# Performance work log

Measured on AMD Instinct MI355X. Metric: run time of the kernel, lower is better.

## Reference

```python
import jax, jax.numpy as jnp
import numpy as np

N_NODES = 100000
N_EDGES = 1600000
D_IN = 264
D_HID = 64
NEG_SLOPE = 0.2


def _glorot(key, shape):
    fan_in, fan_out = shape[0], shape[-1]
    lim = jnp.sqrt(6.0 / (fan_in + fan_out))
    return jax.random.uniform(key, shape, jnp.float32, -lim, lim)


def setup_inputs() -> dict:
    key = jax.random.key(0)
    ks = jax.random.split(key, 24)
    x = jax.random.normal(ks[0], (N_NODES, D_IN), jnp.float32)
    src = jax.random.randint(ks[1], (N_EDGES,), 0, N_NODES, jnp.int32)
    off = jax.random.randint(ks[2], (N_EDGES,), 1, N_NODES, jnp.int32)
    dst = (src + off) % N_NODES  # guaranteed no self loops
    edge_index = jnp.stack([src, dst], axis=0)
    edge_attr = jax.random.normal(ks[3], (N_EDGES, 1), jnp.float32)
    p = {
        'l1_Wl': _glorot(ks[4], (D_IN, D_HID)), 'l1_bl': jnp.zeros((D_HID,), jnp.float32),
        'l1_Wr': _glorot(ks[5], (D_IN, D_HID)), 'l1_br': jnp.zeros((D_HID,), jnp.float32),
        'l1_We': _glorot(ks[6], (1, D_HID)),
        'l1_att': _glorot(ks[7], (1, 1, D_HID)), 'l1_bias': jnp.zeros((D_HID,), jnp.float32),
        'l2_Wl': _glorot(ks[8], (D_HID, D_HID)), 'l2_bl': jnp.zeros((D_HID,), jnp.float32),
        'l2_Wr': _glorot(ks[9], (D_HID, D_HID)), 'l2_br': jnp.zeros((D_HID,), jnp.float32),
        'l2_We': _glorot(ks[10], (1, D_HID)),
        'l2_att': _glorot(ks[11], (1, 1, D_HID)), 'l2_bias': jnp.zeros((D_HID,), jnp.float32),
        'W3': _glorot(ks[12], (D_HID, D_HID)), 'b3': jnp.zeros((D_HID,), jnp.float32),
        'W4': _glorot(ks[13], (D_HID, 1)), 'b4': jnp.zeros((1,), jnp.float32),
    }
    return dict(x=x, edge_index=edge_index, edge_attr=edge_attr, **p)


def _gatv2_layer(x, src, dst, ea, Wl, bl, Wr, br, We, att, bias):
    # heads=1, concat=True, aggr='max' (passed via **kwargs to MessagePassing)
    n = x.shape[0]
    xl = (x @ Wl + bl).reshape(n, 1, D_HID)  # source-side transform
    xr = (x @ Wr + br).reshape(n, 1, D_HID)  # target-side transform
    e = (ea @ We).reshape(-1, 1, D_HID)      # lin_edge, no bias
    m = jax.nn.leaky_relu(xr[dst] + xl[src] + e, NEG_SLOPE)  # (Etot,1,64)
    logits = jnp.sum(m * att, axis=-1)       # (Etot,1)
    # segment softmax over destination nodes
    mx = jax.ops.segment_max(logits, dst, num_segments=n)
    ex = jnp.exp(logits - mx[dst])
    den = jax.ops.segment_sum(ex, dst, num_segments=n)
    alpha = ex / den[dst]                    # (Etot,1)
    msg = xl[src] * alpha[:, :, None]        # (Etot,1,64)
    out = jax.ops.segment_max(msg, dst, num_segments=n)  # aggr='max'
    return out.reshape(n, D_HID) + bias


def _gcn_forward(x, src, dst, edge_attr,
                 l1_Wl, l1_bl, l1_Wr, l1_br, l1_We, l1_att, l1_bias,
                 l2_Wl, l2_bl, l2_Wr, l2_br, l2_We, l2_att, l2_bias,
                 W3, b3, W4, b4):
    n = x.shape[0]
    # add_self_loops with fill_value='mean' (edges contain no self loops)
    loop = jnp.arange(n, dtype=src.dtype)
    src2 = jnp.concatenate([src, loop])
    dst2 = jnp.concatenate([dst, loop])
    mean_ea = jnp.mean(edge_attr, axis=0, keepdims=True)  # (1,1)
    ea2 = jnp.concatenate([edge_attr, jnp.broadcast_to(mean_ea, (n, 1))], axis=0)
    h = _gatv2_layer(x, src2, dst2, ea2, l1_Wl, l1_bl, l1_Wr, l1_br, l1_We, l1_att, l1_bias)
    h = jax.nn.relu(h)  # dropout inactive in eval
    h = _gatv2_layer(h, src2, dst2, ea2, l2_Wl, l2_bl, l2_Wr, l2_br, l2_We, l2_att, l2_bias)
    h = jax.nn.relu(h)
    h = jax.nn.relu(h @ W3 + b3)
    h = h @ W4 + b4
    return jnp.squeeze(h, axis=-1)  # (N,)


def reference(x, edge_index, edge_attr,
              l1_Wl, l1_bl, l1_Wr, l1_br, l1_We, l1_att, l1_bias,
              l2_Wl, l2_bl, l2_Wr, l2_br, l2_We, l2_att, l2_bias,
              W3, b3, W4, b4):
    src, dst = edge_index[0], edge_index[1]
    return _gcn_forward(x, src, dst, edge_attr,
                        l1_Wl, l1_bl, l1_Wr, l1_br, l1_We, l1_att, l1_bias,
                        l2_Wl, l2_bl, l2_Wr, l2_br, l2_We, l2_att, l2_bias,
                        W3, b3, W4, b4)
```

## Files before the change

kernel.cpp:

```cpp
#include <hip/hip_runtime.h>
#include <math.h>
#include <float.h>

#define NN 100000
#define NE 1600000
#define ETOT 1700000
#define DIN 264
#define DH 64
#define SLOPE 0.2f
#define NB 98

typedef __attribute__((ext_vector_type(8))) short s8v;
typedef __attribute__((ext_vector_type(4))) float f4v;

__device__ __forceinline__ unsigned short f2bf(float x) {
  unsigned u = __float_as_uint(x);
  u += 0x7FFFu + ((u >> 16) & 1u);
  return (unsigned short)(u >> 16);
}
__device__ __forceinline__ float bf2f(unsigned short h) {
  return __uint_as_float(((unsigned)h) << 16);
}

__global__ void k_mean(const float* __restrict__ ea, float* __restrict__ sum) {
  float acc = 0.f;
  for (int i = blockIdx.x * blockDim.x + threadIdx.x; i < NE; i += gridDim.x * blockDim.x)
    acc += ea[i];
  #pragma unroll
  for (int off = 32; off > 0; off >>= 1) acc += __shfl_xor(acc, off);
  __shared__ float s[4];
  int lane = threadIdx.x & 63, w = threadIdx.x >> 6;
  if (lane == 0) s[w] = acc;
  __syncthreads();
  if (threadIdx.x == 0) atomicAdd(sum, s[0] + s[1] + s[2] + s[3]);
}

__global__ void k_hist(const int* __restrict__ ei, unsigned* __restrict__ deg) {
  int e = blockIdx.x * blockDim.x + threadIdx.x;
  if (e >= ETOT) return;
  int d = (e < NE) ? ei[NE + e] : e - NE;
  atomicAdd(&deg[d], 1u);
}

__global__ __launch_bounds__(256)
void k_bsum(const unsigned* __restrict__ deg, unsigned* __restrict__ bsum) {
  int i0 = blockIdx.x * 1024 + threadIdx.x * 4;
  unsigned s = 0;
  if (i0 + 3 < NN) {
    uint4 v = *(const uint4*)&deg[i0];
    s = v.x + v.y + v.z + v.w;
  }
  #pragma unroll
  for (int off = 32; off > 0; off >>= 1) s += __shfl_xor(s, off);
  __shared__ unsigned ws[4];
  int lane = threadIdx.x & 63, w = threadIdx.x >> 6;
  if (lane == 0) ws[w] = s;
  __syncthreads();
  if (threadIdx.x == 0) bsum[blockIdx.x] = ws[0] + ws[1] + ws[2] + ws[3];
}

__global__ __launch_bounds__(128)
void k_sscan(unsigned* __restrict__ bsum, unsigned* __restrict__ rowptr) {
  __shared__ unsigned ls[128];
  int t = threadIdx.x;
  unsigned v = (t < NB) ? bsum[t] : 0u;
  ls[t] = v;
  __syncthreads();
  for (int off = 1; off < 128; off <<= 1) {
    unsigned u = (t >= off) ? ls[t - off] : 0u;
    __syncthreads();
    ls[t] += u;
    __syncthreads();
  }
  if (t < NB) bsum[t] = ls[t] - v;
  if (t == 127) rowptr[NN] = ls[127];
}

__global__ __launch_bounds__(256)
void k_scan2(const unsigned* __restrict__ deg, const unsigned* __restrict__ bsum,
             unsigned* __restrict__ rowptr, unsigned* __restrict__ wptr) {
  __shared__ unsigned ls[256];
  int i0 = blockIdx.x * 1024 + threadIdx.x * 4;
  unsigned d0 = 0, d1 = 0, d2 = 0, d3 = 0;
  if (i0 + 3 < NN) {
    uint4 v = *(const uint4*)&deg[i0];
    d0 = v.x; d1 = v.y; d2 = v.z; d3 = v.w;
  }
  unsigned ts = d0 + d1 + d2 + d3;
  ls[threadIdx.x] = ts;
  __syncthreads();
  for (int off = 1; off < 256; off <<= 1) {
    unsigned u = (threadIdx.x >= (unsigned)off) ? ls[threadIdx.x - off] : 0u;
    __syncthreads();
    ls[threadIdx.x] += u;
    __syncthreads();
  }
  unsigned base = bsum[blockIdx.x] + ls[threadIdx.x] - ts;
  if (i0 + 3 < NN) {
    uint4 r;
    r.x = base;
    r.y = base + d0;
    r.z = r.y + d1;
    r.w = r.z + d2;
    *(uint4*)&rowptr[i0] = r;
    *(uint4*)&wptr[i0] = r;
  }
}

__global__ void k_scatter(const int* __restrict__ ei, const float* __restrict__ ea,
                          const float* __restrict__ sump, unsigned* __restrict__ wptr,
                          int2* __restrict__ csr) {
  int e = blockIdx.x * blockDim.x + threadIdx.x;
  if (e >= ETOT) return;
  int s, d;
  float a;
  if (e < NE) {
    s = ei[e];
    d = ei[NE + e];
    a = ea[e];
  } else {
    s = d = e - NE;
    a = sump[0] * (1.0f / NE);
  }
  unsigned pos = atomicAdd(&wptr[d], 1u);
  csr[pos] = make_int2(s, __float_as_int(a));
}

template <int K>
__global__ __launch_bounds__(256)
void k_wprep(const float* __restrict__ Wl, const float* __restrict__ Wr,
             unsigned short* __restrict__ wfh, unsigned short* __restrict__ wfl) {
  constexpr int KC = (K + 31) / 32;
  int t = blockIdx.x * blockDim.x + threadIdx.x;
  if (t >= 8 * KC * 64) return;
  int lane = t & 63;
  int kc = (t >> 6) % KC;
  int ntg = t / (64 * KC);
  const float* src = (ntg < 4) ? Wl : Wr;
  int n = (ntg & 3) * 16 + (lane & 15);
  int k0 = kc * 32 + (lane >> 4) * 8;
  #pragma unroll
  for (int i = 0; i < 8; i++) {
    int k = k0 + i;
    float v = (k < K) ? src[k * DH + n] : 0.f;
    unsigned short hh = f2bf(v);
    wfh[t * 8 + i] = hh;
    wfl[t * 8 + i] = f2bf(v - bf2f(hh));
  }
}

template <int K>
__global__ __launch_bounds__(512) __attribute__((amdgpu_waves_per_eu(4)))
void k_mm(const float* __restrict__ X,
          const unsigned short* __restrict__ wfh, const unsigned short* __restrict__ wfl,
          const float* __restrict__ bl, const float* __restrict__ br,
          float* __restrict__ xl, float* __restrict__ xr) {
  constexpr int KC = (K + 31) / 32;
  constexpr int KP = KC * 32;
  constexpr int SP = KP + 8;
  __shared__ unsigned short lsh[64 * SP];
  __shared__ unsigned short lsl[64 * SP];
  const int r0 = blockIdx.x * 64;
  const int tid = threadIdx.x;
  const int lane = tid & 63, w = tid >> 6;
  const int kq = lane >> 4;
  const int ar = lane & 15;

  s8v bh[KC], bv[KC];
  #pragma unroll
  for (int kc = 0; kc < KC; kc++) {
    const int bidx = ((w * KC + kc) * 64 + lane) * 8;
    bh[kc] = *(const s8v*)&wfh[bidx];
    bv[kc] = *(const s8v*)&wfl[bidx];
  }

  if constexpr (KP > K) {
    constexpr int PADW = (KP - K) / 2;
    for (int t = tid; t < 64 * PADW; t += 512) {
      int row = t / PADW, c = t - row * PADW;
      *(unsigned*)&lsh[row * SP + K + 2 * c] = 0u;
      *(unsigned*)&lsl[row * SP + K + 2 * c] = 0u;
    }
  }
  {
    constexpr int HK = K / 2;
    for (int p = tid; p < 64 * HK; p += 512) {
      int row = p / HK, kp = p - row * HK;
      int grow = r0 + row;
      float a = 0.f, b = 0.f;
      if (grow < NN) {
        float2 v = *(const float2*)&X[(size_t)grow * K + 2 * kp];
        a = v.x; b = v.y;
      }
      unsigned short ha = f2bf(a), hb = f2bf(b);
      unsigned short la = f2bf(a - bf2f(ha)), lb = f2bf(b - bf2f(hb));
      *(unsigned*)&lsh[row * SP + 2 * kp] = (unsigned)ha | ((unsigned)hb << 16);
      *(unsigned*)&lsl[row * SP + 2 * kp] = (unsigned)la | ((unsigned)lb << 16);
    }
  }
  __syncthreads();

  f4v acc[4];
  #pragma unroll
  for (int mt = 0; mt < 4; mt++) acc[mt] = (f4v){0.f, 0.f, 0.f, 0.f};
  #pragma unroll
  for (int kc = 0; kc < KC; kc++) {
    const int kb = kc * 32 + kq * 8;
    #pragma unroll
    for (int mt = 0; mt < 4; mt++) {
      s8v ah = *(const s8v*)&lsh[(mt * 16 + ar) * SP + kb];
      s8v al = *(const s8v*)&lsl[(mt * 16 + ar) * SP + kb];
      acc[mt] = __builtin_amdgcn_mfma_f32_16x16x32_bf16(ah, bh[kc], acc[mt], 0, 0, 0);
      acc[mt] = __builtin_amdgcn_mfma_f32_16x16x32_bf16(ah, bv[kc], acc[mt], 0, 0, 0);
      acc[mt] = __builtin_amdgcn_mfma_f32_16x16x32_bf16(al, bh[kc], acc[mt], 0, 0, 0);
    }
  }

  const float* bias = (w < 4) ? bl : br;
  float* outp = (w < 4) ? xl : xr;
  const int col = (w & 3) * 16 + ar;
  const float bvv = bias[col];
  #pragma unroll
  for (int mt = 0; mt < 4; mt++) {
    #pragma unroll
    for (int r = 0; r < 4; r++) {
      int grow = r0 + mt * 16 + kq * 4 + r;
      if (grow < NN) outp[(size_t)grow * DH + col] = acc[mt][r] + bvv;
    }
  }
}

template <bool HEAD>
__global__ void k_attn(const unsigned* __restrict__ rowptr, const int2* __restrict__ csr,
                       const float* __restrict__ xl, const float* __restrict__ xr,
                       const float* __restrict__ We, const float* __restrict__ att,
                       const float* __restrict__ bias, float* __restrict__ h,
                       const float* __restrict__ W3, const float* __restrict__ b3,
                       const float* __restrict__ W4, const float* __restrict__ b4,
                       float* __restrict__ out) {
  int n = (blockIdx.x * blockDim.x + threadIdx.x) >> 4;
  int l = threadIdx.x & 15;
  int g0 = threadIdx.x & 48;
  if (n >= NN) return;
  int l4 = l * 4;
  float4 xr4 = *(const float4*)&xr[n * DH + l4];
  float4 we4 = *(const float4*)&We[l4];
  float4 at4 = *(const float4*)&att[l4];
  int beg = rowptr[n], end = rowptr[n + 1];
  float M, D;
  float4 V;
  {
    int2 c0 = csr[beg];
    float a = __int_as_float(c0.y);
    float4 sl = *(const float4*)&xl[c0.x * DH + l4];
    float v, p = 0.f;
    v = xr4.x + sl.x + a * we4.x; v = v > 0.f ? v : SLOPE * v; p += v * at4.x;
    v = xr4.y + sl.y + a * we4.y; v = v > 0.f ? v : SLOPE * v; p += v * at4.y;
    v = xr4.z + sl.z + a * we4.z; v = v > 0.f ? v : SLOPE * v; p += v * at4.z;
    v = xr4.w + sl.w + a * we4.w; v = v > 0.f ? v : SLOPE * v; p += v * at4.w;
    p += __shfl_xor(p, 1);
    p += __shfl_xor(p, 2);
    p += __shfl_xor(p, 4);
    p += __shfl_xor(p, 8);
    M = p; D = 1.f; V = sl;
  }
  for (int e0 = beg + 1; e0 < end; e0 += 16) {
    int2 cl = csr[min(e0 + l, end - 1)];
    int cnt = min(16, end - e0);
    for (int i = 0; i < cnt; i += 4) {
      int mm = min(4, cnt - i);
      float4 sl[4];
      float av[4];
      #pragma unroll
      for (int j = 0; j < 4; j++) {
        if (j < mm) {
          int s = __shfl(cl.x, g0 + i + j);
          av[j] = __int_as_float(__shfl(cl.y, g0 + i + j));
          sl[j] = *(const float4*)&xl[s * DH + l4];
        }
      }
      #pragma unroll
      for (int j = 0; j < 4; j++) {
        if (j < mm) {
          float a = av[j];
          float v, p = 0.f;
          v = xr4.x + sl[j].x + a * we4.x; v = v > 0.f ? v : SLOPE * v; p += v * at4.x;
          v = xr4.y + sl[j].y + a * we4.y; v = v > 0.f ? v : SLOPE * v; p += v * at4.y;
          v = xr4.z + sl[j].z + a * we4.z; v = v > 0.f ? v : SLOPE * v; p += v * at4.z;
          v = xr4.w + sl[j].w + a * we4.w; v = v > 0.f ? v : SLOPE * v; p += v * at4.w;
          p += __shfl_xor(p, 1);
          p += __shfl_xor(p, 2);
          p += __shfl_xor(p, 4);
          p += __shfl_xor(p, 8);
          float Mn = fmaxf(M, p);
          float sO = __expf(M - Mn), sN = __expf(p - Mn);
          D = D * sO + sN;
          V.x = fmaxf(V.x * sO, sl[j].x * sN);
          V.y = fmaxf(V.y * sO, sl[j].y * sN);
          V.z = fmaxf(V.z * sO, sl[j].z * sN);
          V.w = fmaxf(V.w * sO, sl[j].w * sN);
          M = Mn;
        }
      }
    }
  }
  float inv = 1.0f / D;
  float4 b = *(const float4*)&bias[l4];
  float4 o;
  o.x = fmaxf(V.x * inv + b.x, 0.f);
  o.y = fmaxf(V.y * inv + b.y, 0.f);
  o.z = fmaxf(V.z * inv + b.z, 0.f);
  o.w = fmaxf(V.w * inv + b.w, 0.f);
  if (!HEAD) {
    *(float4*)&h[n * DH + l4] = o;
  } else {
    float4 acc = {0.f, 0.f, 0.f, 0.f};
    #pragma unroll
    for (int kk = 0; kk < 16; kk++) {
      float4 hk;
      hk.x = __shfl(o.x, g0 + kk);
      hk.y = __shfl(o.y, g0 + kk);
      hk.z = __shfl(o.z, g0 + kk);
      hk.w = __shfl(o.w, g0 + kk);
      float4 w0 = *(const float4*)&W3[(kk * 4 + 0) * DH + l4];
      acc.x = fmaf(hk.x, w0.x, acc.x);
      acc.y = fmaf(hk.x, w0.y, acc.y);
      acc.z = fmaf(hk.x, w0.z, acc.z);
      acc.w = fmaf(hk.x, w0.w, acc.w);
      float4 w1 = *(const float4*)&W3[(kk * 4 + 1) * DH + l4];
      acc.x = fmaf(hk.y, w1.x, acc.x);
      acc.y = fmaf(hk.y, w1.y, acc.y);
      acc.z = fmaf(hk.y, w1.z, acc.z);
      acc.w = fmaf(hk.y, w1.w, acc.w);
      float4 w2 = *(const float4*)&W3[(kk * 4 + 2) * DH + l4];
      acc.x = fmaf(hk.z, w2.x, acc.x);
      acc.y = fmaf(hk.z, w2.y, acc.y);
      acc.z = fmaf(hk.z, w2.z, acc.z);
      acc.w = fmaf(hk.z, w2.w, acc.w);
      float4 w3 = *(const float4*)&W3[(kk * 4 + 3) * DH + l4];
      acc.x = fmaf(hk.w, w3.x, acc.x);
      acc.y = fmaf(hk.w, w3.y, acc.y);
      acc.z = fmaf(hk.w, w3.z, acc.z);
      acc.w = fmaf(hk.w, w3.w, acc.w);
    }
    float4 b3v = *(const float4*)&b3[l4];
    float4 w4v = *(const float4*)&W4[l4];
    float t, p = 0.f;
    t = acc.x + b3v.x; t = t > 0.f ? t : 0.f; p += t * w4v.x;
    t = acc.y + b3v.y; t = t > 0.f ? t : 0.f; p += t * w4v.y;
    t = acc.z + b3v.z; t = t > 0.f ? t : 0.f; p += t * w4v.z;
    t = acc.w + b3v.w; t = t > 0.f ? t : 0.f; p += t * w4v.w;
    p += __shfl_xor(p, 1);
    p += __shfl_xor(p, 2);
    p += __shfl_xor(p, 4);
    p += __shfl_xor(p, 8);
    if (l == 0) out[n] = p + b4[0];
  }
}

extern "C" void kernel_launch(void* const* d_in, const int* in_sizes, int n_in,
                              void* d_out, int out_size, void* d_ws, size_t ws_size,
                              hipStream_t stream) {
  const float* x      = (const float*)d_in[0];
  const int*   ei     = (const int*)d_in[1];
  const float* ea     = (const float*)d_in[2];
  const float* l1_Wl  = (const float*)d_in[3];
  const float* l1_bl  = (const float*)d_in[4];
  const float* l1_Wr  = (const float*)d_in[5];
  const float* l1_br  = (const float*)d_in[6];
  const float* l1_We  = (const float*)d_in[7];
  const float* l1_att = (const float*)d_in[8];
  const float* l1_bias= (const float*)d_in[9];
  const float* l2_Wl  = (const float*)d_in[10];
  const float* l2_bl  = (const float*)d_in[11];
  const float* l2_Wr  = (const float*)d_in[12];
  const float* l2_br  = (const float*)d_in[13];
  const float* l2_We  = (const float*)d_in[14];
  const float* l2_att = (const float*)d_in[15];
  const float* l2_bias= (const float*)d_in[16];
  const float* W3     = (const float*)d_in[17];
  const float* b3     = (const float*)d_in[18];
  const float* W4     = (const float*)d_in[19];
  const float* b4     = (const float*)d_in[20];
  float* out = (float*)d_out;

  float*    ws     = (float*)d_ws;
  float*    sum    = ws;
  float*    xl     = ws + 256;
  float*    xr     = xl + NN * DH;
  float*    h      = xr + NN * DH;
  int2*     csr    = (int2*)(h + NN * DH);
  unsigned* rowptr = (unsigned*)(csr + ETOT);
  unsigned* wptr   = rowptr + NN + 4;
  unsigned* deg    = wptr + NN;
  unsigned* bsum   = deg + NN;
  unsigned short* wf1h = (unsigned short*)(bsum + 128);
  unsigned short* wf1l = wf1h + 36864;
  unsigned short* wf2h = wf1l + 36864;
  unsigned short* wf2l = wf2h + 8192;

  const int B = 256;
  const int mm_blocks   = (NN + 63) / 64;
  const int edge_blocks = (ETOT + B - 1) / B;
  const int attn_blocks = (NN * 16) / B;

  hipMemsetAsync(sum, 0, 256 * sizeof(float), stream);
  hipMemsetAsync(deg, 0, NN * sizeof(unsigned), stream);
  k_wprep<DIN><<<(8 * 9 * 64 + B - 1) / B, B, 0, stream>>>(l1_Wl, l1_Wr, wf1h, wf1l);
  k_wprep<DH><<<(8 * 2 * 64 + B - 1) / B, B, 0, stream>>>(l2_Wl, l2_Wr, wf2h, wf2l);
  k_mean<<<256, B, 0, stream>>>(ea, sum);
  k_hist<<<edge_blocks, B, 0, stream>>>(ei, deg);
  k_bsum<<<NB, B, 0, stream>>>(deg, bsum);
  k_sscan<<<1, 128, 0, stream>>>(bsum, rowptr);
  k_scan2<<<NB, B, 0, stream>>>(deg, bsum, rowptr, wptr);
  k_scatter<<<edge_blocks, B, 0, stream>>>(ei, ea, sum, wptr, csr);

  k_mm<DIN><<<mm_blocks, 512, 0, stream>>>(x, wf1h, wf1l, l1_bl, l1_br, xl, xr);
  k_attn<false><<<attn_blocks, B, 0, stream>>>(rowptr, csr, xl, xr, l1_We, l1_att,
                                               l1_bias, h, W3, b3, W4, b4, out);

  k_mm<DH><<<mm_blocks, 512, 0, stream>>>(h, wf2h, wf2l, l2_bl, l2_br, xl, xr);
  k_attn<true><<<attn_blocks, B, 0, stream>>>(rowptr, csr, xl, xr, l2_We, l2_att,
                                              l2_bias, h, W3, b3, W4, b4, out);
}
```

Measured before the change: 661.9 us.

## Shard histogram and CSR scatter atomics by destination range across blocks

The histogram and scatter kernels now launch NSHARD copies of each edge chunk. Each block handles only the destinations in its shard's node range, and blockIdx.x interleaves the shards. The aim is to confine the atomics from concurrently running blocks to separate address ranges, improving L2 locality and spreading atomic contention on MI355X's partitioned caches. In exchange, every block reads the destination indices eight times, and most threads do no work after filtering.

```diff
diff --git a/kernel.cpp b/kernel.cpp
--- a/kernel.cpp
+++ b/kernel.cpp
@@ -9,6 +9,9 @@
 #define DH 64
 #define SLOPE 0.2f
 #define NB 98
+#define NSHARD 8
+#define SHW 12500
+#define EPB 2048
 
 typedef __attribute__((ext_vector_type(8))) short s8v;
 typedef __attribute__((ext_vector_type(4))) float f4v;
@@ -35,11 +38,20 @@
   if (threadIdx.x == 0) atomicAdd(sum, s[0] + s[1] + s[2] + s[3]);
 }
 
-__global__ void k_hist(const int* __restrict__ ei, unsigned* __restrict__ deg) {
-  int e = blockIdx.x * blockDim.x + threadIdx.x;
-  if (e >= ETOT) return;
-  int d = (e < NE) ? ei[NE + e] : e - NE;
-  atomicAdd(&deg[d], 1u);
+__global__ __launch_bounds__(256)
+void k_hist(const int* __restrict__ ei, unsigned* __restrict__ deg) {
+  const int shard = blockIdx.x & (NSHARD - 1);
+  const int g = blockIdx.x >> 3;
+  const int dlo = shard * SHW, dhi = dlo + SHW;
+  int e0 = g * EPB + threadIdx.x;
+  #pragma unroll
+  for (int k = 0; k < EPB / 256; k++) {
+    int e = e0 + k * 256;
+    if (e < ETOT) {
+      int d = (e < NE) ? ei[NE + e] : e - NE;
+      if (d >= dlo && d < dhi) atomicAdd(&deg[d], 1u);
+    }
+  }
 }
 
 __global__ __launch_bounds__(256)
@@ -107,23 +119,32 @@
   }
 }
 
-__global__ void k_scatter(const int* __restrict__ ei, const float* __restrict__ ea,
-                          const float* __restrict__ sump, unsigned* __restrict__ wptr,
-                          int2* __restrict__ csr) {
-  int e = blockIdx.x * blockDim.x + threadIdx.x;
-  if (e >= ETOT) return;
-  int s, d;
-  float a;
-  if (e < NE) {
-    s = ei[e];
-    d = ei[NE + e];
-    a = ea[e];
-  } else {
-    s = d = e - NE;
-    a = sump[0] * (1.0f / NE);
-  }
-  unsigned pos = atomicAdd(&wptr[d], 1u);
-  csr[pos] = make_int2(s, __float_as_int(a));
+__global__ __launch_bounds__(256)
+void k_scatter(const int* __restrict__ ei, const float* __restrict__ ea,
+               const float* __restrict__ sump, unsigned* __restrict__ wptr,
+               int2* __restrict__ csr) {
+  const int shard = blockIdx.x & (NSHARD - 1);
+  const int g = blockIdx.x >> 3;
+  const int dlo = shard * SHW, dhi = dlo + SHW;
+  int e0 = g * EPB + threadIdx.x;
+  #pragma unroll
+  for (int k = 0; k < EPB / 256; k++) {
+    int e = e0 + k * 256;
+    if (e >= ETOT) continue;
+    int d = (e < NE) ? ei[NE + e] : e - NE;
+    if (d < dlo || d >= dhi) continue;
+    int s;
+    float a;
+    if (e < NE) {
+      s = ei[e];
+      a = ea[e];
+    } else {
+      s = d;
+      a = sump[0] * (1.0f / NE);
+    }
+    unsigned pos = atomicAdd(&wptr[d], 1u);
+    csr[pos] = make_int2(s, __float_as_int(a));
+  }
 }
 
 template <int K>
@@ -401,7 +422,7 @@
 
   const int B = 256;
   const int mm_blocks   = (NN + 63) / 64;
-  const int edge_blocks = (ETOT + B - 1) / B;
+  const int shard_blocks = NSHARD * ((ETOT + EPB - 1) / EPB);
   const int attn_blocks = (NN * 16) / B;
 
   hipMemsetAsync(sum, 0, 256 * sizeof(float), stream);
@@ -409,11 +430,11 @@
   k_wprep<DIN><<<(8 * 9 * 64 + B - 1) / B, B, 0, stream>>>(l1_Wl, l1_Wr, wf1h, wf1l);
   k_wprep<DH><<<(8 * 2 * 64 + B - 1) / B, B, 0, stream>>>(l2_Wl, l2_Wr, wf2h, wf2l);
   k_mean<<<256, B, 0, stream>>>(ea, sum);
-  k_hist<<<edge_blocks, B, 0, stream>>>(ei, deg);
+  k_hist<<<shard_blocks, B, 0, stream>>>(ei, deg);
   k_bsum<<<NB, B, 0, stream>>>(deg, bsum);
   k_sscan<<<1, 128, 0, stream>>>(bsum, rowptr);
   k_scan2<<<NB, B, 0, stream>>>(deg, bsum, rowptr, wptr);
-  k_scatter<<<edge_blocks, B, 0, stream>>>(ei, ea, sum, wptr, csr);
+  k_scatter<<<shard_blocks, B, 0, stream>>>(ei, ea, sum, wptr, csr);
 
   k_mm<DIN><<<mm_blocks, 512, 0, stream>>>(x, wf1h, wf1l, l1_bl, l1_br, xl, xr);
   k_attn<false><<<attn_blocks, B, 0, stream>>>(rowptr, csr, xl, xr, l1_We, l1_att,
```

Result: faster. 617.7 us (-6.7%).
